# Performance work log

Measured on AMD Instinct MI355X. Metric: run time of the kernel, lower is better.

The kernel has to match this reference:

```python
import jax, jax.numpy as jnp
import numpy as np

N = 20000          # nodes
E = 320000         # edges (avg degree 16)
D_IN, D1, D2, D_OUT = 256, 512, 256, 64
EPS = 1e-5


def _glorot(key, shape):
    lim = (6.0 / (shape[0] + shape[1])) ** 0.5
    return jax.random.uniform(key, shape, jnp.float32, -lim, lim)


def setup_inputs() -> dict:
    key = jax.random.key(0)
    ks = jax.random.split(key, 8)
    x = jax.random.normal(ks[0], (N, D_IN), jnp.float32)
    edge_index = jax.random.randint(ks[1], (2, E), 0, N, dtype=jnp.int64)
    return {
        "x": x,
        "edge_index": edge_index,
        # SAGEConv 1 (SoftmaxAggregation temperature t1 over inp_dim channels)
        "t1": jnp.ones((1, D_IN), jnp.float32),
        "Wl1": _glorot(ks[2], (D_IN, D1)), "bl1": jnp.zeros((D1,), jnp.float32),
        "Wr1": _glorot(ks[3], (D_IN, D1)),
        "g1": jnp.ones((D1,), jnp.float32), "beta1": jnp.zeros((D1,), jnp.float32),
        # SAGEConv 2
        "t2": jnp.ones((1, D1), jnp.float32),
        "Wl2": _glorot(ks[4], (D1, D2)), "bl2": jnp.zeros((D2,), jnp.float32),
        "Wr2": _glorot(ks[5], (D1, D2)),
        "g2": jnp.ones((D2,), jnp.float32), "beta2": jnp.zeros((D2,), jnp.float32),
        # final linear + LayerNorm
        "Wf": _glorot(ks[6], (D2, D_OUT)), "bf": jnp.zeros((D_OUT,), jnp.float32),
        "gx": jnp.ones((D_OUT,), jnp.float32), "betax": jnp.zeros((D_OUT,), jnp.float32),
    }


def _sage_softmax(x, src, dst, t, Wl, bl, Wr, n):
    """SAGEConv with learnable per-channel SoftmaxAggregation."""
    m = x[src]                                              # [E, C] gathered messages
    a = m * t                                               # scaled logits
    amax = jax.ops.segment_max(a, dst, num_segments=n)      # [N, C]
    e = jnp.exp(a - amax[dst])
    denom = jax.ops.segment_sum(e, dst, num_segments=n)     # [N, C]
    w = e / denom[dst]                                      # segment softmax weights
    agg = jax.ops.segment_sum(m * w, dst, num_segments=n)   # weighted neighbor sum
    return agg @ Wl + bl + x @ Wr


def _graph_ln(x, g, b):
    # PyG LayerNorm mode='graph', batch=None: normalize over ALL nodes & channels
    mu = x.mean()
    std = jnp.sqrt(((x - mu) ** 2).mean())
    return (x - mu) / (std + EPS) * g + b


def _ln(x, g, b):
    mu = x.mean(-1, keepdims=True)
    var = ((x - mu) ** 2).mean(-1, keepdims=True)
    return (x - mu) / jnp.sqrt(var + EPS) * g + b


def reference(x, edge_index, t1, Wl1, bl1, Wr1, g1, beta1,
              t2, Wl2, bl2, Wr2, g2, beta2, Wf, bf, gx, betax):
    src, dst = edge_index[0], edge_index[1]
    h = _sage_softmax(x, src, dst, t1, Wl1, bl1, Wr1, N)
    h = jax.nn.relu(_graph_ln(h, g1, beta1))
    h = _sage_softmax(h, src, dst, t2, Wl2, bl2, Wr2, N)
    h = jax.nn.relu(_graph_ln(h, g2, beta2))
    p = h.mean(0, keepdims=True)                            # global_mean_pool, batch=None -> [1, 256]
    out = _ln(p @ Wf + bf, gx, betax)
    return jax.nn.relu(out)
```

## Files before the change

### kernel.cpp

```cpp
#include <hip/hip_runtime.h>
#include <math.h>

#define NODES 20000
#define MPAD  20096
#define EDGES 320000
#define EPSV  1e-5f
#define LOG2E 1.4426950408889634f

#define PREP_CNT   1250
#define PREP_CAST  5000
#define PREP_TR    512
#define PREP_TOTAL (PREP_CNT + PREP_CAST + PREP_TR + 1)

typedef short bf16x8 __attribute__((ext_vector_type(8)));
typedef float f32x4  __attribute__((ext_vector_type(4)));

__device__ __forceinline__ unsigned short f2bf(float f) {
    unsigned int u = __float_as_uint(f);
    u = (u + 0x7fffu + ((u >> 16) & 1u)) >> 16;
    return (unsigned short)u;
}
__device__ __forceinline__ float bf2f(unsigned short h) {
    return __uint_as_float(((unsigned int)h) << 16);
}

__device__ __forceinline__ void load_lds16(const unsigned short* g, unsigned short* l) {
    __builtin_amdgcn_global_load_lds(
        (const __attribute__((address_space(1))) unsigned int*)g,
        (__attribute__((address_space(3))) unsigned int*)l, 16, 0, 0);
}

__global__ void k_prep(const int* __restrict__ dst, int* __restrict__ counts,
                       const float* __restrict__ x, unsigned short* __restrict__ xb,
                       const float* __restrict__ Wl1, const float* __restrict__ Wr1,
                       const float* __restrict__ Wl2, const float* __restrict__ Wr2,
                       unsigned short* __restrict__ o1l, unsigned short* __restrict__ o1r,
                       unsigned short* __restrict__ o2l, unsigned short* __restrict__ o2r,
                       float* __restrict__ acc, float* __restrict__ colsum) {
    int b = blockIdx.x;
    int t = threadIdx.x;
    if (b < PREP_CNT) {
        int e = b * 256 + t;
        if (e < EDGES) atomicAdd(&counts[dst[e]], 1);
    } else if (b < PREP_CNT + PREP_CAST) {
        int i = ((b - PREP_CNT) * 256 + t) * 4;
        float4 v = *(const float4*)(x + i);
        xb[i + 0] = f2bf(v.x); xb[i + 1] = f2bf(v.y);
        xb[i + 2] = f2bf(v.z); xb[i + 3] = f2bf(v.w);
    } else if (b < PREP_CNT + PREP_CAST + PREP_TR) {
        __shared__ float tile[32][33];
        int zz = b - PREP_CNT - PREP_CAST;
        int z = zz >> 7;
        int idx = zz & 127;
        const float* W = (z == 0) ? Wl1 : (z == 1) ? Wr1 : (z == 2) ? Wl2 : Wr2;
        unsigned short* Wt = (z == 0) ? o1l : (z == 1) ? o1r : (z == 2) ? o2l : o2r;
        int K = (z < 2) ? 256 : 512, N = (z < 2) ? 512 : 256;
        int nb = N / 32;
        int n0 = (idx % nb) * 32, k0 = (idx / nb) * 32;
        int tx = t & 31, ty = t >> 5;
#pragma unroll
        for (int j = 0; j < 4; j++)
            tile[ty + j * 8][tx] = W[(size_t)(k0 + ty + j * 8) * N + n0 + tx];
        __syncthreads();
#pragma unroll
        for (int j = 0; j < 4; j++)
            Wt[(size_t)(n0 + ty + j * 8) * K + k0 + tx] = f2bf(tile[tx][ty + j * 8]);
    } else {
        if (t < 4) acc[t] = 0.f;
        colsum[t] = 0.f;
    }
}

__global__ void k_scan(const int* __restrict__ counts, int* __restrict__ offs) {
    __shared__ int ssum[256];
    int t = threadIdx.x;
    const int chunk = (NODES + 255) / 256;
    int b = t * chunk, e = b + chunk;
    if (b > NODES) b = NODES;
    if (e > NODES) e = NODES;
    int s = 0;
    for (int i = b; i < e; i++) s += counts[i];
    ssum[t] = s;
    __syncthreads();
    int v = s;
#pragma unroll
    for (int o = 1; o < 256; o <<= 1) {
        int add = (t >= o) ? ssum[t - o] : 0;
        __syncthreads();
        v += add;
        ssum[t] = v;
        __syncthreads();
    }
    int run = v - s;
    if (t == 255) offs[NODES] = v;
    for (int i = b; i < e; i++) { offs[i] = run; run += counts[i]; }
}

__global__ void k_scatter(const int* __restrict__ src, const int* __restrict__ dst,
                          const int* __restrict__ offs, int* __restrict__ cursor,
                          int* __restrict__ csr_src) {
    int e = blockIdx.x * blockDim.x + threadIdx.x;
    if (e < EDGES) {
        int d = dst[e];
        int pos = atomicAdd(&cursor[d], 1);
        csr_src[offs[d] + pos] = src[e];
    }
}

template <int C, int S, int UNR>
__global__ void k_agg_s(const unsigned short* __restrict__ xb, const float* __restrict__ tt,
                        const int* __restrict__ offs, const int* __restrict__ csr,
                        unsigned short* __restrict__ out) {
    static_assert(C / S == 64, "one channel per lane");
    int t = threadIdx.x;
    int lane = t & 63;
    int slice = blockIdx.x % S;
    int node = (blockIdx.x / S) * 4 + (t >> 6);
    if (node >= NODES) return;
    int beg = __builtin_amdgcn_readfirstlane(offs[node]);
    int end = __builtin_amdgcn_readfirstlane(offs[node + 1]);
    int c = slice * 64 + lane;
    const unsigned short* __restrict__ xc = xb + c;
    float tl = tt[c] * LOG2E;
    float l = 0.f, s = 0.f;
    int k = beg;
    for (; k + UNR <= end; k += UNR) {
        float xv[UNR];
#pragma unroll
        for (int u = 0; u < UNR; u++) {
            int sn = csr[k + u];
            xv[u] = bf2f(xc[(size_t)sn * C]);
        }
#pragma unroll
        for (int u = 0; u < UNR; u++) {
            float p = __builtin_amdgcn_exp2f(xv[u] * tl);
            l += p;
            s = fmaf(p, xv[u], s);
        }
    }
    for (; k < end; k++) {
        int sn = csr[k];
        float xv = bf2f(xc[(size_t)sn * C]);
        float p = __builtin_amdgcn_exp2f(xv * tl);
        l += p;
        s = fmaf(p, xv, s);
    }
    out[(size_t)node * C + c] = f2bf(end > beg ? s / l : 0.f);
}

template <int K, int NT>
__global__ __launch_bounds__(256) void k_gemm_mfma(
    const unsigned short* __restrict__ A1, const unsigned short* __restrict__ B1t,
    const unsigned short* __restrict__ A2, const unsigned short* __restrict__ B2t,
    const float* __restrict__ bias, unsigned short* __restrict__ Co, int M,
    float* __restrict__ stat) {
    __shared__ short As[128 * 32];
    __shared__ short Bs[128 * 32];
    __shared__ float rs[256], rq[256];

    int t = threadIdx.x;
    int m0 = blockIdx.x * 128, n0 = blockIdx.y * 128;
    int wv = t >> 6, lane = t & 63;
    int wm = wv & 1, wn = wv >> 1;
    int lm = lane & 15, quad = lane >> 4;
    int sr = t >> 2;
    int sc8 = (t & 3) * 8;

    f32x4 acc[4][4] = {};

    for (int ph = 0; ph < 2; ph++) {
        const unsigned short* __restrict__ A  = ph ? A2 : A1;
        const unsigned short* __restrict__ Bt = ph ? B2t : B1t;
        for (int k0 = 0; k0 < K; k0 += 32) {
#pragma unroll
            for (int it = 0; it < 2; it++) {
                load_lds16(A  + (size_t)(m0 + it * 64 + sr) * K + k0 + sc8,
                           (unsigned short*)&As[it * 2048 + wv * 512]);
                load_lds16(Bt + (size_t)(n0 + it * 64 + sr) * K + k0 + sc8,
                           (unsigned short*)&Bs[it * 2048 + wv * 512]);
            }
            __syncthreads();
            bf16x8 af[4], bfr[4];
#pragma unroll
            for (int i = 0; i < 4; i++) {
                af[i]  = *(const bf16x8*)&As[(wm * 64 + i * 16 + lm) * 32 + quad * 8];
                bfr[i] = *(const bf16x8*)&Bs[(wn * 64 + i * 16 + lm) * 32 + quad * 8];
            }
#pragma unroll
            for (int mi = 0; mi < 4; mi++)
#pragma unroll
                for (int nj = 0; nj < 4; nj++)
                    acc[mi][nj] = __builtin_amdgcn_mfma_f32_16x16x32_bf16(
                        af[mi], bfr[nj], acc[mi][nj], 0, 0, 0);
            __syncthreads();
        }
    }

    float sum = 0.f, ss = 0.f;
#pragma unroll
    for (int mi = 0; mi < 4; mi++) {
        int rb = m0 + wm * 64 + mi * 16 + quad * 4;
#pragma unroll
        for (int nj = 0; nj < 4; nj++) {
            int col = n0 + wn * 64 + nj * 16 + lm;
            float bb = bias[col];
#pragma unroll
            for (int rg = 0; rg < 4; rg++) {
                int row = rb + rg;
                if (row < M) {
                    float y = acc[mi][nj][rg] + bb;
                    Co[(size_t)row * NT + col] = f2bf(y);
                    sum += y; ss += y * y;
                }
            }
        }
    }
    rs[t] = sum; rq[t] = ss;
    __syncthreads();
    for (int o = 128; o > 0; o >>= 1) {
        if (t < o) { rs[t] += rs[t + o]; rq[t] += rq[t + o]; }
        __syncthreads();
    }
    if (t == 0) { atomicAdd(&stat[0], rs[0]); atomicAdd(&stat[1], rq[0]); }
}

template <int C>
__global__ void k_ln_relu_b(unsigned short* __restrict__ h, int n,
                            const float* __restrict__ st,
                            const float* __restrict__ g, const float* __restrict__ b) {
    typedef unsigned short us8 __attribute__((ext_vector_type(8)));
    float mu = st[0] / (float)n;
    float var = st[1] / (float)n - mu * mu;
    var = var < 0.f ? 0.f : var;
    float inv = 1.0f / (sqrtf(var) + EPSV);
    int i8 = (blockIdx.x * blockDim.x + threadIdx.x) * 8;
    if (i8 >= n) return;
    int c = i8 & (C - 1);
    us8 v = *(const us8*)(h + i8);
    us8 o;
#pragma unroll
    for (int j = 0; j < 8; j++) {
        float y = (bf2f(v[j]) - mu) * inv * g[c + j] + b[c + j];
        o[j] = f2bf(fmaxf(y, 0.f));
    }
    *(us8*)(h + i8) = o;
}

__global__ void k_ln_colsum(const unsigned short* __restrict__ h, int n,
                            const float* __restrict__ st,
                            const float* __restrict__ g, const float* __restrict__ b,
                            float* __restrict__ colsum) {
    float mu = st[0] / (float)n;
    float var = st[1] / (float)n - mu * mu;
    var = var < 0.f ? 0.f : var;
    float inv = 1.0f / (sqrtf(var) + EPSV);
    int t = threadIdx.x;
    float gv = g[t], bv = b[t];
    float local = 0.f;
    int stride = gridDim.x * blockDim.x;
    for (int i = blockIdx.x * blockDim.x + t; i < n; i += stride) {
        float y = (bf2f(h[i]) - mu) * inv * gv + bv;
        local += fmaxf(y, 0.f);
    }
    atomicAdd(&colsum[t], local);
}

__global__ void k_final(const float* __restrict__ colsum, const float* __restrict__ Wf,
                        const float* __restrict__ bf, const float* __restrict__ gx,
                        const float* __restrict__ bx, float* __restrict__ out) {
    __shared__ float p[256];
    int t = threadIdx.x;
    p[t] = colsum[t] * (1.0f / (float)NODES);
    __syncthreads();
    if (t < 64) {
        float acc = bf[t];
        for (int c = 0; c < 256; c++) acc = fmaf(p[c], Wf[c * 64 + t], acc);
        float sum = acc;
        for (int o = 32; o > 0; o >>= 1) sum += __shfl_xor(sum, o);
        float mu = sum * (1.0f / 64.0f);
        float d = acc - mu;
        float vs = d * d;
        for (int o = 32; o > 0; o >>= 1) vs += __shfl_xor(vs, o);
        float var = vs * (1.0f / 64.0f);
        float y = d * rsqrtf(var + EPSV) * gx[t] + bx[t];
        out[t] = fmaxf(y, 0.f);
    }
}

extern "C" void kernel_launch(void* const* d_in, const int* in_sizes, int n_in,
                              void* d_out, int out_size, void* d_ws, size_t ws_size,
                              hipStream_t stream) {
    const float* x   = (const float*)d_in[0];
    const int*   ei  = (const int*)d_in[1];
    const float* t1  = (const float*)d_in[2];
    const float* Wl1 = (const float*)d_in[3];
    const float* bl1 = (const float*)d_in[4];
    const float* Wr1 = (const float*)d_in[5];
    const float* g1  = (const float*)d_in[6];
    const float* be1 = (const float*)d_in[7];
    const float* t2  = (const float*)d_in[8];
    const float* Wl2 = (const float*)d_in[9];
    const float* bl2 = (const float*)d_in[10];
    const float* Wr2 = (const float*)d_in[11];
    const float* g2  = (const float*)d_in[12];
    const float* be2 = (const float*)d_in[13];
    const float* Wf  = (const float*)d_in[14];
    const float* bf  = (const float*)d_in[15];
    const float* gx  = (const float*)d_in[16];
    const float* bx  = (const float*)d_in[17];
    float* out = (float*)d_out;

    char* ws = (char*)d_ws;
    size_t off = 0;
    auto alloc = [&](size_t bytes) { size_t o = off; off = (off + bytes + 511) & ~511ull; return o; };
    size_t o_counts = alloc((size_t)NODES * 4);
    size_t o_cursor = alloc((size_t)NODES * 4);
    size_t zero_bytes = off;
    size_t o_acc    = alloc(4 * 4);
    size_t o_colsum = alloc(256 * 4);
    size_t o_offs = alloc((size_t)(NODES + 1) * 4);
    size_t o_csrc = alloc((size_t)EDGES * 4);
    size_t o_w1l  = alloc((size_t)512 * 256 * 2);
    size_t o_w1r  = alloc((size_t)512 * 256 * 2);
    size_t o_w2l  = alloc((size_t)256 * 512 * 2);
    size_t o_w2r  = alloc((size_t)256 * 512 * 2);
    size_t o_bufX = alloc((size_t)MPAD * 256 * 2);
    size_t o_agg  = alloc((size_t)MPAD * 512 * 2);
    size_t o_h1   = alloc((size_t)MPAD * 512 * 2);

    int*   counts = (int*)(ws + o_counts);
    int*   cursor = (int*)(ws + o_cursor);
    float* acc    = (float*)(ws + o_acc);
    float* colsum = (float*)(ws + o_colsum);
    int*   offs   = (int*)(ws + o_offs);
    int*   csrc   = (int*)(ws + o_csrc);
    unsigned short* w1lt = (unsigned short*)(ws + o_w1l);
    unsigned short* w1rt = (unsigned short*)(ws + o_w1r);
    unsigned short* w2lt = (unsigned short*)(ws + o_w2l);
    unsigned short* w2rt = (unsigned short*)(ws + o_w2r);
    unsigned short* xb   = (unsigned short*)(ws + o_bufX);
    unsigned short* h2p  = (unsigned short*)(ws + o_bufX);
    unsigned short* aggb = (unsigned short*)(ws + o_agg);
    unsigned short* h1   = (unsigned short*)(ws + o_h1);

    const int* src = ei;
    const int* dst = ei + EDGES;

    hipMemsetAsync(ws, 0, zero_bytes, stream);

    k_prep<<<PREP_TOTAL, 256, 0, stream>>>(dst, counts, x, xb,
                                           Wl1, Wr1, Wl2, Wr2,
                                           w1lt, w1rt, w2lt, w2rt,
                                           acc, colsum);
    k_scan<<<1, 256, 0, stream>>>(counts, offs);
    k_scatter<<<(EDGES + 255) / 256, 256, 0, stream>>>(src, dst, offs, cursor, csrc);

    k_agg_s<256, 4, 8><<<(NODES / 4) * 4, 256, 0, stream>>>(xb, t1, offs, csrc, aggb);
    k_gemm_mfma<256, 512><<<dim3(MPAD / 128, 4), 256, 0, stream>>>(
        aggb, w1lt, xb, w1rt, bl1, h1, NODES, acc);
    k_ln_relu_b<512><<<NODES * 512 / 8 / 256, 256, 0, stream>>>(h1, NODES * 512, acc, g1, be1);

    k_agg_s<512, 8, 8><<<(NODES / 4) * 8, 256, 0, stream>>>(h1, t2, offs, csrc, aggb);
    k_gemm_mfma<512, 256><<<dim3(MPAD / 128, 2), 256, 0, stream>>>(
        aggb, w2lt, h1, w2rt, bl2, h2p, NODES, acc + 2);

    k_ln_colsum<<<1024, 256, 0, stream>>>(h2p, NODES * 256, acc + 2, g2, be2, colsum);
    k_final<<<1, 256, 0, stream>>>(colsum, Wf, bf, gx, bx, out);
}
```

Measured before the change: 371.5 us.

## Pack two bf16 channels per lane in aggregation and swizzle GEMM block order

The softmax aggregation kernel now has each lane handle two adjacent channels through a single 32-bit load, with packed float2 math. This halves the number of slices and gather instructions per node. The GEMM launch becomes a 1D grid remapped so that groups of 8 M-tiles cycle through all N-tiles, which improves L2 reuse of A rows. The extra guard blocks and the h1 buffer padding cover the rounded-up grid, at the cost of fewer blocks and less parallelism in aggregation.

```diff
diff --git a/kernel.cpp b/kernel.cpp
--- a/kernel.cpp
+++ b/kernel.cpp
@@ -14,6 +14,7 @@
 
 typedef short bf16x8 __attribute__((ext_vector_type(8)));
 typedef float f32x4  __attribute__((ext_vector_type(4)));
+typedef float f2     __attribute__((ext_vector_type(2)));
 
 __device__ __forceinline__ unsigned short f2bf(float f) {
     unsigned int u = __float_as_uint(f);
@@ -108,10 +109,10 @@
 }
 
 template <int C, int S, int UNR>
-__global__ void k_agg_s(const unsigned short* __restrict__ xb, const float* __restrict__ tt,
+__global__ void k_agg_x(const unsigned short* __restrict__ xb, const float* __restrict__ tt,
                         const int* __restrict__ offs, const int* __restrict__ csr,
                         unsigned short* __restrict__ out) {
-    static_assert(C / S == 64, "one channel per lane");
+    static_assert(C / S == 128, "CS must be 128 (VPL=2 packed)");
     int t = threadIdx.x;
     int lane = t & 63;
     int slice = blockIdx.x % S;
@@ -119,36 +120,55 @@
     if (node >= NODES) return;
     int beg = __builtin_amdgcn_readfirstlane(offs[node]);
     int end = __builtin_amdgcn_readfirstlane(offs[node + 1]);
-    int c = slice * 64 + lane;
-    const unsigned short* __restrict__ xc = xb + c;
-    float tl = tt[c] * LOG2E;
-    float l = 0.f, s = 0.f;
+    int cb = slice * 128 + lane * 2;
+    const unsigned short* __restrict__ xcb = xb + cb;
+    f2 tl, l, s;
+    tl[0] = tt[cb] * LOG2E;
+    tl[1] = tt[cb + 1] * LOG2E;
+    l[0] = 0.f; l[1] = 0.f;
+    s[0] = 0.f; s[1] = 0.f;
     int k = beg;
     for (; k + UNR <= end; k += UNR) {
-        float xv[UNR];
+        unsigned d[UNR];
 #pragma unroll
         for (int u = 0; u < UNR; u++) {
             int sn = csr[k + u];
-            xv[u] = bf2f(xc[(size_t)sn * C]);
+            d[u] = *(const unsigned*)(xcb + (size_t)sn * C);
         }
 #pragma unroll
         for (int u = 0; u < UNR; u++) {
-            float p = __builtin_amdgcn_exp2f(xv[u] * tl);
+            unsigned wd = d[u];
+            f2 xv;
+            xv[0] = __uint_as_float(wd << 16);
+            xv[1] = __uint_as_float(wd & 0xffff0000u);
+            f2 a = xv * tl;
+            f2 p;
+            p[0] = __builtin_amdgcn_exp2f(a[0]);
+            p[1] = __builtin_amdgcn_exp2f(a[1]);
             l += p;
-            s = fmaf(p, xv[u], s);
+            s = __builtin_elementwise_fma(p, xv, s);
         }
     }
     for (; k < end; k++) {
         int sn = csr[k];
-        float xv = bf2f(xc[(size_t)sn * C]);
-        float p = __builtin_amdgcn_exp2f(xv * tl);
+        unsigned wd = *(const unsigned*)(xcb + (size_t)sn * C);
+        f2 xv;
+        xv[0] = __uint_as_float(wd << 16);
+        xv[1] = __uint_as_float(wd & 0xffff0000u);
+        f2 a = xv * tl;
+        f2 p;
+        p[0] = __builtin_amdgcn_exp2f(a[0]);
+        p[1] = __builtin_amdgcn_exp2f(a[1]);
         l += p;
-        s = fmaf(p, xv, s);
-    }
-    out[(size_t)node * C + c] = f2bf(end > beg ? s / l : 0.f);
-}
-
-template <int K, int NT>
+        s = __builtin_elementwise_fma(p, xv, s);
+    }
+    bool has = end > beg;
+    unsigned o = (unsigned)f2bf(has ? s[0] / l[0] : 0.f)
+               | ((unsigned)f2bf(has ? s[1] / l[1] : 0.f) << 16);
+    *(unsigned*)(out + (size_t)node * C + cb) = o;
+}
+
+template <int K, int NT, int NTILES>
 __global__ __launch_bounds__(256) void k_gemm_mfma(
     const unsigned short* __restrict__ A1, const unsigned short* __restrict__ B1t,
     const unsigned short* __restrict__ A2, const unsigned short* __restrict__ B2t,
@@ -158,8 +178,14 @@
     __shared__ short Bs[128 * 32];
     __shared__ float rs[256], rq[256];
 
-    int t = threadIdx.x;
-    int m0 = blockIdx.x * 128, n0 = blockIdx.y * 128;
+    int bx = blockIdx.x;
+    int xid = bx & 7, q = bx >> 3;
+    int n = q % NTILES, mh = q / NTILES;
+    int m = mh * 8 + xid;
+    if (m * 128 >= MPAD) return;
+    int m0 = m * 128, n0 = n * 128;
+
+    int t = threadIdx.x;
     int wv = t >> 6, lane = t & 63;
     int wm = wv & 1, wn = wv >> 1;
     int lm = lane & 15, quad = lane >> 4;
@@ -326,7 +352,7 @@
     size_t o_w2r  = alloc((size_t)256 * 512 * 2);
     size_t o_bufX = alloc((size_t)MPAD * 256 * 2);
     size_t o_agg  = alloc((size_t)MPAD * 512 * 2);
-    size_t o_h1   = alloc((size_t)MPAD * 512 * 2);
+    size_t o_h1   = alloc((size_t)(MPAD + 512) * 512 * 2);
 
     int*   counts = (int*)(ws + o_counts);
     int*   cursor = (int*)(ws + o_cursor);
@@ -355,13 +381,13 @@
     k_scan<<<1, 256, 0, stream>>>(counts, offs);
     k_scatter<<<(EDGES + 255) / 256, 256, 0, stream>>>(src, dst, offs, cursor, csrc);
 
-    k_agg_s<256, 4, 8><<<(NODES / 4) * 4, 256, 0, stream>>>(xb, t1, offs, csrc, aggb);
-    k_gemm_mfma<256, 512><<<dim3(MPAD / 128, 4), 256, 0, stream>>>(
+    k_agg_x<256, 2, 8><<<(NODES / 4) * 2, 256, 0, stream>>>(xb, t1, offs, csrc, aggb);
+    k_gemm_mfma<256, 512, 4><<<8 * 4 * 20, 256, 0, stream>>>(
         aggb, w1lt, xb, w1rt, bl1, h1, NODES, acc);
     k_ln_relu_b<512><<<NODES * 512 / 8 / 256, 256, 0, stream>>>(h1, NODES * 512, acc, g1, be1);
 
-    k_agg_s<512, 8, 8><<<(NODES / 4) * 8, 256, 0, stream>>>(h1, t2, offs, csrc, aggb);
-    k_gemm_mfma<512, 256><<<dim3(MPAD / 128, 2), 256, 0, stream>>>(
+    k_agg_x<512, 4, 8><<<(NODES / 4) * 4, 256, 0, stream>>>(h1, t2, offs, csrc, aggb);
+    k_gemm_mfma<512, 256, 2><<<8 * 2 * 20, 256, 0, stream>>>(
         aggb, w2lt, h1, w2rt, bl2, h2p, NODES, acc + 2);
 
     k_ln_colsum<<<1024, 256, 0, stream>>>(h2p, NODES * 256, acc + 2, g2, be2, colsum);
```

After: 346.0 us. -6.8%, faster.
